# Optimization experiments

Measured on AMD Instinct MI355X. Metric: run time of the kernel, lower is better.

Reference implementation:

```python
import jax, jax.numpy as jnp
import numpy as np

HEADS = 16
DIM = 1024


def setup_inputs() -> dict:
    key = jax.random.key(0)
    ks = jax.random.split(key, 9)
    B, N, D = 2, 2048, DIM
    s = 1.0 / np.sqrt(D)
    x = jax.random.normal(ks[0], (B, N, D), dtype=jnp.float32)
    Wq = jax.random.normal(ks[1], (D, D), dtype=jnp.float32) * s
    Wk = jax.random.normal(ks[2], (D, D), dtype=jnp.float32) * s
    Wv = jax.random.normal(ks[3], (D, D), dtype=jnp.float32) * s
    Wo = jax.random.normal(ks[4], (D, D), dtype=jnp.float32) * s
    bq = jax.random.normal(ks[5], (D,), dtype=jnp.float32) * 0.01
    bk = jax.random.normal(ks[6], (D,), dtype=jnp.float32) * 0.01
    bv = jax.random.normal(ks[7], (D,), dtype=jnp.float32) * 0.01
    bo = jax.random.normal(ks[8], (D,), dtype=jnp.float32) * 0.01
    return {"x": x, "Wq": Wq, "bq": bq, "Wk": Wk, "bk": bk,
            "Wv": Wv, "bv": bv, "Wo": Wo, "bo": bo}


def reference(x, Wq, bq, Wk, bk, Wv, bv, Wo, bo):
    B, N, D = x.shape
    H = HEADS
    hd = D // H
    scale = hd ** (-0.5)
    # projections; split heads -> [B, H, N, hd]
    q = (x @ Wq + bq).reshape(B, N, H, hd).transpose(0, 2, 1, 3)
    k = (x @ Wk + bk).reshape(B, N, H, hd).transpose(0, 2, 1, 3)
    v = (x @ Wv + bv).reshape(B, N, H, hd).transpose(0, 2, 1, 3)
    # full [B, H, N, N] scores (faithful to naive torch implementation)
    attn = jnp.einsum('bhqd,bhkd->bhqk', q, k) * scale
    attn = jax.nn.softmax(attn, axis=-1)
    # dropout is identity in eval mode
    out = jnp.einsum('bhqk,bhkd->bhqd', attn, v)
    out = out.transpose(0, 2, 1, 3).reshape(B, N, D)
    return out @ Wo + bo
```

## Files before the change

kernel.cpp:

```cpp
#include <hip/hip_runtime.h>

#define HEADS 16
#define HD 64
#define SEQ 2048
#define DMODEL 1024
#define BATCH 2
#define MTOT (BATCH*SEQ)
#define KVB 64
#define NKH 16

typedef unsigned short u16;
typedef __bf16 bf16;
typedef bf16 bf16x8 __attribute__((ext_vector_type(8)));
typedef float f32x4 __attribute__((ext_vector_type(4)));
typedef float f32x16 __attribute__((ext_vector_type(16)));
typedef unsigned short u16x8 __attribute__((ext_vector_type(8)));
typedef unsigned short u16x4 __attribute__((ext_vector_type(4)));

static __device__ __forceinline__ u16 f2bf(float f) {
  bf16 b = (bf16)f;
  return __builtin_bit_cast(u16, b);
}

static __device__ __forceinline__ void async16(u16* lds_base, const u16* g) {
  __builtin_amdgcn_global_load_lds(
      (const __attribute__((address_space(1))) unsigned int*)g,
      (__attribute__((address_space(3))) unsigned int*)lds_base,
      16, 0, 0);
}

__global__ __launch_bounds__(256) void k_cvt(const float* __restrict__ in,
                                             u16* __restrict__ out, int n8) {
  int i = blockIdx.x * blockDim.x + threadIdx.x;
  if (i >= n8) return;
  const float4* p = (const float4*)(in + (size_t)i * 8);
  float4 a = p[0], b = p[1];
  u16x8 r;
  r[0] = f2bf(a.x); r[1] = f2bf(a.y); r[2] = f2bf(a.z); r[3] = f2bf(a.w);
  r[4] = f2bf(b.x); r[5] = f2bf(b.y); r[6] = f2bf(b.z); r[7] = f2bf(b.w);
  *(u16x8*)(out + (size_t)i * 8) = r;
}

__global__ __launch_bounds__(256) void k_cvtT(const float* __restrict__ W0, const float* __restrict__ W1,
                                              const float* __restrict__ W2, const float* __restrict__ W3,
                                              u16* __restrict__ T0, u16* __restrict__ T1,
                                              u16* __restrict__ T2, u16* __restrict__ T3) {
  const float* W = blockIdx.z == 0 ? W0 : blockIdx.z == 1 ? W1 : blockIdx.z == 2 ? W2 : W3;
  u16*         T = blockIdx.z == 0 ? T0 : blockIdx.z == 1 ? T1 : blockIdx.z == 2 ? T2 : T3;
  __shared__ u16 tile[64 * 68];
  int t = threadIdx.x;
  int kb = blockIdx.y * 64, nb = blockIdx.x * 64;
#pragma unroll
  for (int i = 0; i < 4; ++i) {
    int c = t * 4 + i;
    int row = c >> 4;
    int c4 = c & 15;
    float4 v = *(const float4*)&W[(size_t)(kb + row) * DMODEL + nb + c4 * 4];
    tile[row * 68 + c4 * 4 + 0] = f2bf(v.x);
    tile[row * 68 + c4 * 4 + 1] = f2bf(v.y);
    tile[row * 68 + c4 * 4 + 2] = f2bf(v.z);
    tile[row * 68 + c4 * 4 + 3] = f2bf(v.w);
  }
  __syncthreads();
#pragma unroll
  for (int i = 0; i < 2; ++i) {
    int c = t * 2 + i;
    int n = c >> 3;
    int k8 = c & 7;
    u16x8 v;
#pragma unroll
    for (int e = 0; e < 8; ++e) v[e] = tile[(k8 * 8 + e) * 68 + n];
    *(u16x8*)&T[(size_t)(nb + n) * DMODEL + kb + k8 * 8] = v;
  }
}

__global__ __launch_bounds__(256) void k_gemm(
    const u16* __restrict__ A,
    const u16* __restrict__ BT0, const u16* __restrict__ BT1, const u16* __restrict__ BT2,
    const float* __restrict__ b0, const float* __restrict__ b1, const float* __restrict__ b2,
    void* __restrict__ O0, void* __restrict__ O1, void* __restrict__ O2,
    int M, int N, int K) {
  const u16* BT = blockIdx.z == 0 ? BT0 : blockIdx.z == 1 ? BT1 : BT2;
  const float* bias = blockIdx.z == 0 ? b0 : blockIdx.z == 1 ? b1 : b2;
  void* Out = blockIdx.z == 0 ? O0 : blockIdx.z == 1 ? O1 : O2;

  __shared__ u16 Ads[2][128 * 32];
  __shared__ u16 Bds[2][128 * 32];
  int tid = threadIdx.x, wid = tid >> 6, lane = tid & 63;
  int r = lane & 15, g = lane >> 4;
  int wm = wid >> 1, wn = wid & 1;
  int m0 = blockIdx.y * 128, n0 = blockIdx.x * 128;

  f32x4 acc[4][4];
  f32x4 zero4 = {0.f, 0.f, 0.f, 0.f};
#pragma unroll
  for (int mt = 0; mt < 4; ++mt)
#pragma unroll
    for (int nt = 0; nt < 4; ++nt) acc[mt][nt] = zero4;

  int srow = lane >> 2;
  int scb = lane & 3;

  auto STAGE = [&](int b, int k0) {
#pragma unroll
    for (int tt = 0; tt < 2; ++tt) {
      int inst = wid * 2 + tt;
      int row = inst * 16 + srow;
      async16(&Ads[b][inst * 512], &A[(size_t)(m0 + row) * K + k0 + scb * 8]);
      async16(&Bds[b][inst * 512], &BT[(size_t)(n0 + row) * K + k0 + scb * 8]);
    }
  };

  auto BODY = [&](int buf, int k0) {
    if (k0 + 32 < K) STAGE(buf ^ 1, k0 + 32);
    bf16x8 af[4], bfv[4];
#pragma unroll
    for (int mt = 0; mt < 4; ++mt)
      af[mt] = *(const bf16x8*)&Ads[buf][(wm * 64 + mt * 16 + r) * 32 + g * 8];
#pragma unroll
    for (int nt = 0; nt < 4; ++nt)
      bfv[nt] = *(const bf16x8*)&Bds[buf][(wn * 64 + nt * 16 + r) * 32 + g * 8];
#pragma unroll
    for (int mt = 0; mt < 4; ++mt)
#pragma unroll
      for (int nt = 0; nt < 4; ++nt)
        acc[mt][nt] = __builtin_amdgcn_mfma_f32_16x16x32_bf16(af[mt], bfv[nt], acc[mt][nt], 0, 0, 0);
    asm volatile("s_waitcnt vmcnt(0)" ::: "memory");
    __builtin_amdgcn_sched_barrier(0);
    __builtin_amdgcn_s_barrier();
    __builtin_amdgcn_sched_barrier(0);
  };

  STAGE(0, 0);
  asm volatile("s_waitcnt vmcnt(0)" ::: "memory");
  __builtin_amdgcn_sched_barrier(0);
  __builtin_amdgcn_s_barrier();
  __builtin_amdgcn_sched_barrier(0);

  for (int k0 = 0; k0 < K; k0 += 64) {
    BODY(0, k0);
    BODY(1, k0 + 32);
  }

  const float qs = 0.18033688011112042f;
#pragma unroll
  for (int nt = 0; nt < 4; ++nt) {
    int col = n0 + wn * 64 + nt * 16 + r;
    float bv = bias[col];
#pragma unroll
    for (int mt = 0; mt < 4; ++mt) {
      int rowb = m0 + wm * 64 + mt * 16 + g * 4;
      int b = rowb >> 11;
      int h = col >> 6, d = col & (HD - 1);
      if (blockIdx.z == 2) {
        int n = rowb & (SEQ - 1);
        int np = (n & ~12) | ((n & 4) << 1) | ((n & 8) >> 1);
        u16x4 pk;
#pragma unroll
        for (int j = 0; j < 4; ++j) pk[j] = f2bf(acc[mt][nt][j] + bv);
        *(u16x4*)&((u16*)Out)[((size_t)((b * HEADS + h) * HD + d)) * SEQ + np] = pk;
      } else {
        float sc = (blockIdx.z == 0) ? qs : 1.0f;
#pragma unroll
        for (int j = 0; j < 4; ++j) {
          int row = rowb + j;
          int n = row & (SEQ - 1);
          ((u16*)Out)[((size_t)(b * HEADS + h) * SEQ + n) * HD + d] = f2bf((acc[mt][nt][j] + bv) * sc);
        }
      }
    }
  }
}

__global__ __launch_bounds__(512, 2) void k_gemm1(
    const u16* __restrict__ A, const u16* __restrict__ BT,
    const float* __restrict__ bias, float* __restrict__ Out,
    int M, int N, int K) {
  __shared__ u16 smem[32768];
  u16* Apart = smem;
  u16* Bpart = smem + 16384;

  int tid = threadIdx.x, wid = tid >> 6, lane = tid & 63;
  int r = lane & 15, g = lane >> 4;
  int h = wid >> 2, w = wid & 3;
  int wm = w >> 1, wn = w & 1;

  int fid = blockIdx.y * gridDim.x + blockIdx.x;
  int nb = (fid & 7) * 32 + (fid >> 3);
  int m0 = (nb >> 3) * 128, n0 = (nb & 7) * 128;

  f32x4 acc[4][4];
  f32x4 zero4 = {0.f, 0.f, 0.f, 0.f};
#pragma unroll
  for (int mt = 0; mt < 4; ++mt)
#pragma unroll
    for (int nt = 0; nt < 4; ++nt) acc[mt][nt] = zero4;

  int srow = lane >> 2;
  int scb = lane & 3;
  const int KH = K >> 1;

  auto STAGE = [&](int b, int k0) {
    int kg = h * KH + k0;
#pragma unroll
    for (int tt = 0; tt < 2; ++tt) {
      int inst = w * 2 + tt;
      int row = inst * 16 + srow;
      async16(&Apart[((b * 2 + h) * 8 + inst) * 512], &A[(size_t)(m0 + row) * K + kg + scb * 8]);
      async16(&Bpart[((b * 2 + h) * 8 + inst) * 512], &BT[(size_t)(n0 + row) * K + kg + scb * 8]);
    }
  };

  auto BODY = [&](int buf, int k0) {
    if (k0 + 32 < KH) STAGE(buf ^ 1, k0 + 32);
    const u16* Ab = &Apart[(buf * 2 + h) * 4096];
    const u16* Bb = &Bpart[(buf * 2 + h) * 4096];
    bf16x8 af[4], bfv[4];
#pragma unroll
    for (int mt = 0; mt < 4; ++mt)
      af[mt] = *(const bf16x8*)&Ab[(wm * 64 + mt * 16 + r) * 32 + g * 8];
#pragma unroll
    for (int nt = 0; nt < 4; ++nt)
      bfv[nt] = *(const bf16x8*)&Bb[(wn * 64 + nt * 16 + r) * 32 + g * 8];
#pragma unroll
    for (int mt = 0; mt < 4; ++mt)
#pragma unroll
      for (int nt = 0; nt < 4; ++nt)
        acc[mt][nt] = __builtin_amdgcn_mfma_f32_16x16x32_bf16(af[mt], bfv[nt], acc[mt][nt], 0, 0, 0);
    asm volatile("s_waitcnt vmcnt(0)" ::: "memory");
    __builtin_amdgcn_sched_barrier(0);
    __builtin_amdgcn_s_barrier();
    __builtin_amdgcn_sched_barrier(0);
  };

  STAGE(0, 0);
  asm volatile("s_waitcnt vmcnt(0)" ::: "memory");
  __builtin_amdgcn_sched_barrier(0);
  __builtin_amdgcn_s_barrier();
  __builtin_amdgcn_sched_barrier(0);

  for (int k0 = 0; k0 < KH; k0 += 64) {
    BODY(0, k0);
    BODY(1, k0 + 32);
  }

  __syncthreads();
  float* cfp = (float*)smem;
  if (h == 1) {
#pragma unroll
    for (int mt = 0; mt < 4; ++mt)
#pragma unroll
      for (int nt = 0; nt < 4; ++nt)
#pragma unroll
        for (int j = 0; j < 4; ++j)
          cfp[(wm * 64 + mt * 16 + g * 4 + j) * 128 + wn * 64 + nt * 16 + r] = acc[mt][nt][j];
  }
  __syncthreads();
  if (h == 0) {
#pragma unroll
    for (int nt = 0; nt < 4; ++nt) {
      int col = n0 + wn * 64 + nt * 16 + r;
      float bv = bias[col];
#pragma unroll
      for (int mt = 0; mt < 4; ++mt) {
        int rowb = m0 + wm * 64 + mt * 16 + g * 4;
#pragma unroll
        for (int j = 0; j < 4; ++j) {
          float v = acc[mt][nt][j] + bv +
                    cfp[(wm * 64 + mt * 16 + g * 4 + j) * 128 + wn * 64 + nt * 16 + r];
          Out[(size_t)(rowb + j) * N + col] = v;
        }
      }
    }
  }
}

__global__ __launch_bounds__(512, 2) void k_attn(const u16* __restrict__ Q,
                                                 const u16* __restrict__ Kg,
                                                 const u16* __restrict__ Vt,
                                                 u16* __restrict__ Oa) {
  __shared__ u16 lds[2][2][2][KVB * 64];

  int tid = threadIdx.x, wid = tid >> 6, lane = tid & 63;
  int l31 = lane & 31, hi = lane >> 5;
  int h = wid >> 2, s = wid & 3;

  int fid = blockIdx.y * gridDim.x + blockIdx.x;
  int swz = (fid & 7) * 32 + (fid >> 3);
  int qt = swz & 7;
  int bh = swz >> 3;

  const size_t kbase = (size_t)bh * SEQ * HD;
  const size_t vbase = (size_t)bh * HD * SEQ;
  int qA = qt * 256 + s * 64;

  bf16x8 qfA[4], qfB[4];
#pragma unroll
  for (int db = 0; db < 4; ++db) {
    qfA[db] = *(const bf16x8*)&Q[kbase + (size_t)(qA + l31) * HD + db * 16 + hi * 8];
    qfB[db] = *(const bf16x8*)&Q[kbase + (size_t)(qA + 32 + l31) * HD + db * 16 + hi * 8];
  }

  int swz7 = l31 & 7;
  int coff[4];
#pragma unroll
  for (int i = 0; i < 4; ++i) coff[i] = ((2 * i + hi) ^ swz7) * 8;

  f32x16 zero16 = {0.f,0.f,0.f,0.f,0.f,0.f,0.f,0.f,0.f,0.f,0.f,0.f,0.f,0.f,0.f,0.f};
  f32x16 oa0A = zero16, oa1A = zero16, lA = zero16;
  f32x16 oa0B = zero16, oa1B = zero16, lB = zero16;

  u16x8 onesb;
#pragma unroll
  for (int e = 0; e < 8; ++e) onesb[e] = 0x3F80;
  bf16x8 ones = __builtin_bit_cast(bf16x8, onesb);

  auto STAGE = [&](int b, int kc) {
    int kof = (h * NKH + kc) * KVB;
#pragma unroll
    for (int i = 0; i < 2; ++i) {
      int inst = s * 2 + i;
      int rr = inst * 8 + (lane >> 3);
      int ch = (lane & 7) ^ (rr & 7);
      async16(&lds[b][h][0][inst * 512], &Kg[kbase + (size_t)(kof + rr) * HD + ch * 8]);
      async16(&lds[b][h][1][inst * 512], &Vt[vbase + (size_t)rr * SEQ + kof + ch * 8]);
    }
  };

  auto BODY = [&](int buf, int kc) {
    if (kc + 1 < NKH) STAGE(buf ^ 1, kc + 1);

    const u16* Kb = &lds[buf][h][0][0];
    const u16* Vb = &lds[buf][h][1][0];

    f32x16 s0A = zero16, s1A = zero16, s0B = zero16, s1B = zero16;
#pragma unroll
    for (int db = 0; db < 4; ++db) {
      bf16x8 kf0 = *(const bf16x8*)&Kb[l31 * 64 + coff[db]];
      bf16x8 kf1 = *(const bf16x8*)&Kb[2048 + l31 * 64 + coff[db]];
      s0A = __builtin_amdgcn_mfma_f32_32x32x16_bf16(kf0, qfA[db], s0A, 0, 0, 0);
      s1A = __builtin_amdgcn_mfma_f32_32x32x16_bf16(kf1, qfA[db], s1A, 0, 0, 0);
      s0B = __builtin_amdgcn_mfma_f32_32x32x16_bf16(kf0, qfB[db], s0B, 0, 0, 0);
      s1B = __builtin_amdgcn_mfma_f32_32x32x16_bf16(kf1, qfB[db], s1B, 0, 0, 0);
    }

#pragma unroll
    for (int t = 0; t < 4; ++t) {
      u16x8 pkA, pkB;
#pragma unroll
      for (int e = 0; e < 8; ++e) {
        float svA = (t & 2) ? ((t & 1) ? s1A[8 + e] : s1A[e])
                            : ((t & 1) ? s0A[8 + e] : s0A[e]);
        float svB = (t & 2) ? ((t & 1) ? s1B[8 + e] : s1B[e])
                            : ((t & 1) ? s0B[8 + e] : s0B[e]);
        pkA[e] = f2bf(__builtin_amdgcn_exp2f(svA));
        pkB[e] = f2bf(__builtin_amdgcn_exp2f(svB));
      }
      bf16x8 paA = __builtin_bit_cast(bf16x8, pkA);
      bf16x8 paB = __builtin_bit_cast(bf16x8, pkB);

      bf16x8 vf0 = *(const bf16x8*)&Vb[l31 * 64 + coff[t]];
      bf16x8 vf1 = *(const bf16x8*)&Vb[2048 + l31 * 64 + coff[t]];
      lA   = __builtin_amdgcn_mfma_f32_32x32x16_bf16(paA, ones, lA, 0, 0, 0);
      oa0A = __builtin_amdgcn_mfma_f32_32x32x16_bf16(paA, vf0, oa0A, 0, 0, 0);
      oa1A = __builtin_amdgcn_mfma_f32_32x32x16_bf16(paA, vf1, oa1A, 0, 0, 0);
      lB   = __builtin_amdgcn_mfma_f32_32x32x16_bf16(paB, ones, lB, 0, 0, 0);
      oa0B = __builtin_amdgcn_mfma_f32_32x32x16_bf16(paB, vf0, oa0B, 0, 0, 0);
      oa1B = __builtin_amdgcn_mfma_f32_32x32x16_bf16(paB, vf1, oa1B, 0, 0, 0);
    }

    asm volatile("s_waitcnt vmcnt(0)" ::: "memory");
    __builtin_amdgcn_sched_barrier(0);
    __builtin_amdgcn_s_barrier();
    __builtin_amdgcn_sched_barrier(0);
  };

  STAGE(0, 0);
  asm volatile("s_waitcnt vmcnt(0)" ::: "memory");
  __builtin_amdgcn_sched_barrier(0);
  __builtin_amdgcn_s_barrier();
  __builtin_amdgcn_sched_barrier(0);

  for (int kc = 0; kc < NKH; kc += 2) {
    BODY(0, kc);
    BODY(1, kc + 1);
  }

  float* cf = (float*)&lds[0][0][0][0];
  int b = bh >> 4, hh = bh & 15;

  if (h == 1) {
#pragma unroll
    for (int r2 = 0; r2 < 16; ++r2) {
      cf[s * 3072 + r2 * 64 + lane]        = oa0A[r2];
      cf[s * 3072 + 1024 + r2 * 64 + lane] = oa1A[r2];
      cf[s * 3072 + 2048 + r2 * 64 + lane] = lA[r2];
    }
  }
  __syncthreads();
  if (h == 0) {
#pragma unroll
    for (int reg = 0; reg < 16; ++reg) {
      float o0 = oa0A[reg] + cf[s * 3072 + reg * 64 + lane];
      float o1 = oa1A[reg] + cf[s * 3072 + 1024 + reg * 64 + lane];
      float lv = lA[reg]   + cf[s * 3072 + 2048 + reg * 64 + lane];
      float inv = 1.0f / lv;
      int q = qA + (reg & 3) + 8 * (reg >> 2) + 4 * hi;
      size_t rowoff = ((size_t)(b * SEQ + q)) * DMODEL + hh * HD;
      Oa[rowoff + l31]      = f2bf(o0 * inv);
      Oa[rowoff + 32 + l31] = f2bf(o1 * inv);
    }
  }
  __syncthreads();
  if (h == 1) {
#pragma unroll
    for (int r2 = 0; r2 < 16; ++r2) {
      cf[s * 3072 + r2 * 64 + lane]        = oa0B[r2];
      cf[s * 3072 + 1024 + r2 * 64 + lane] = oa1B[r2];
      cf[s * 3072 + 2048 + r2 * 64 + lane] = lB[r2];
    }
  }
  __syncthreads();
  if (h == 0) {
#pragma unroll
    for (int reg = 0; reg < 16; ++reg) {
      float o0 = oa0B[reg] + cf[s * 3072 + reg * 64 + lane];
      float o1 = oa1B[reg] + cf[s * 3072 + 1024 + reg * 64 + lane];
      float lv = lB[reg]   + cf[s * 3072 + 2048 + reg * 64 + lane];
      float inv = 1.0f / lv;
      int q = qA + 32 + (reg & 3) + 8 * (reg >> 2) + 4 * hi;
      size_t rowoff = ((size_t)(b * SEQ + q)) * DMODEL + hh * HD;
      Oa[rowoff + l31]      = f2bf(o0 * inv);
      Oa[rowoff + 32 + l31] = f2bf(o1 * inv);
    }
  }
}

extern "C" void kernel_launch(void* const* d_in, const int* in_sizes, int n_in,
                              void* d_out, int out_size, void* d_ws, size_t ws_size,
                              hipStream_t stream) {
  const float* x  = (const float*)d_in[0];
  const float* Wq = (const float*)d_in[1];
  const float* bq = (const float*)d_in[2];
  const float* Wk = (const float*)d_in[3];
  const float* bk = (const float*)d_in[4];
  const float* Wv = (const float*)d_in[5];
  const float* bv = (const float*)d_in[6];
  const float* Wo = (const float*)d_in[7];
  const float* bo = (const float*)d_in[8];

  char* ws = (char*)d_ws;
  const size_t MB = 1024 * 1024;
  u16* xb    = (u16*)(ws);
  u16* wqT   = (u16*)(ws + 8 * MB);
  u16* wkT   = (u16*)(ws + 10 * MB);
  u16* wvT   = (u16*)(ws + 12 * MB);
  u16* woT   = (u16*)(ws + 14 * MB);
  u16* qbuf  = (u16*)(ws + 16 * MB);
  u16* kbuf  = (u16*)(ws + 24 * MB);
  u16* vbufT = (u16*)(ws + 32 * MB);
  u16* abuf  = (u16*)(ws + 40 * MB);

  k_cvt<<<2048, 256, 0, stream>>>(x, xb, (MTOT * DMODEL) / 8);
  k_cvtT<<<dim3(16, 16, 4), 256, 0, stream>>>(Wq, Wk, Wv, Wo, wqT, wkT, wvT, woT);
  k_gemm<<<dim3(DMODEL / 128, MTOT / 128, 3), 256, 0, stream>>>(
      xb, wqT, wkT, wvT, bq, bk, bv, qbuf, kbuf, vbufT, MTOT, DMODEL, DMODEL);
  k_attn<<<dim3(SEQ / 256, BATCH * HEADS), 512, 0, stream>>>(qbuf, kbuf, vbufT, abuf);
  k_gemm1<<<dim3(DMODEL / 128, MTOT / 128), 512, 0, stream>>>(
      abuf, woT, bo, (float*)d_out, MTOT, DMODEL, DMODEL);
}
```

Baseline: 105.9 us.

## Triple-buffer LDS staging in GEMM and attention kernels with prefetch distance two

Both the projection GEMM and the attention kernel move from double to triple LDS buffers, prefetching two tiles ahead and waiting with vmcnt(4) so the most recent prefetch can stay in flight across the barrier. This is meant to hide global-to-LDS load latency that was previously exposed by a full vmcnt(0) drain every iteration. It raises LDS use, which in the attention kernel (launch bounds 512,2) may reduce occupancy, and the loops now index buffers with mod 3 rather than being unrolled in pairs.

```diff
diff --git a/kernel.cpp b/kernel.cpp
--- a/kernel.cpp
+++ b/kernel.cpp
@@ -27,6 +27,14 @@
       (const __attribute__((address_space(1))) unsigned int*)g,
       (__attribute__((address_space(3))) unsigned int*)lds_base,
       16, 0, 0);
+}
+
+static __device__ __forceinline__ void wait_vm(bool deep) {
+  if (deep) asm volatile("s_waitcnt vmcnt(4)" ::: "memory");
+  else      asm volatile("s_waitcnt vmcnt(0)" ::: "memory");
+  __builtin_amdgcn_sched_barrier(0);
+  __builtin_amdgcn_s_barrier();
+  __builtin_amdgcn_sched_barrier(0);
 }
 
 __global__ __launch_bounds__(256) void k_cvt(const float* __restrict__ in,
@@ -84,8 +92,8 @@
   const float* bias = blockIdx.z == 0 ? b0 : blockIdx.z == 1 ? b1 : b2;
   void* Out = blockIdx.z == 0 ? O0 : blockIdx.z == 1 ? O1 : O2;
 
-  __shared__ u16 Ads[2][128 * 32];
-  __shared__ u16 Bds[2][128 * 32];
+  __shared__ u16 Ads[3][128 * 32];
+  __shared__ u16 Bds[3][128 * 32];
   int tid = threadIdx.x, wid = tid >> 6, lane = tid & 63;
   int r = lane & 15, g = lane >> 4;
   int wm = wid >> 1, wn = wid & 1;
@@ -111,8 +119,8 @@
     }
   };
 
-  auto BODY = [&](int buf, int k0) {
-    if (k0 + 32 < K) STAGE(buf ^ 1, k0 + 32);
+  auto BODY = [&](int buf, int k0, bool deep) {
+    if (k0 + 64 < K) STAGE((buf + 2) % 3, k0 + 64);
     bf16x8 af[4], bfv[4];
 #pragma unroll
     for (int mt = 0; mt < 4; ++mt)
@@ -125,22 +133,16 @@
 #pragma unroll
       for (int nt = 0; nt < 4; ++nt)
         acc[mt][nt] = __builtin_amdgcn_mfma_f32_16x16x32_bf16(af[mt], bfv[nt], acc[mt][nt], 0, 0, 0);
-    asm volatile("s_waitcnt vmcnt(0)" ::: "memory");
-    __builtin_amdgcn_sched_barrier(0);
-    __builtin_amdgcn_s_barrier();
-    __builtin_amdgcn_sched_barrier(0);
+    wait_vm(deep);
   };
 
   STAGE(0, 0);
-  asm volatile("s_waitcnt vmcnt(0)" ::: "memory");
-  __builtin_amdgcn_sched_barrier(0);
-  __builtin_amdgcn_s_barrier();
-  __builtin_amdgcn_sched_barrier(0);
-
-  for (int k0 = 0; k0 < K; k0 += 64) {
-    BODY(0, k0);
-    BODY(1, k0 + 32);
-  }
+  STAGE(1, 32);
+  wait_vm(true);
+
+  int kc = 0;
+  for (int k0 = 0; k0 < K; k0 += 32, ++kc)
+    BODY(kc % 3, k0, k0 + 64 < K);
 
   const float qs = 0.18033688011112042f;
 #pragma unroll
@@ -279,7 +281,7 @@
                                                  const u16* __restrict__ Kg,
                                                  const u16* __restrict__ Vt,
                                                  u16* __restrict__ Oa) {
-  __shared__ u16 lds[2][2][2][KVB * 64];
+  __shared__ u16 lds[3][2][2][KVB * 64];
 
   int tid = threadIdx.x, wid = tid >> 6, lane = tid & 63;
   int l31 = lane & 31, hi = lane >> 5;
@@ -327,8 +329,8 @@
     }
   };
 
-  auto BODY = [&](int buf, int kc) {
-    if (kc + 1 < NKH) STAGE(buf ^ 1, kc + 1);
+  auto BODY = [&](int buf, int kc, bool deep) {
+    if (kc + 2 < NKH) STAGE((buf + 2) % 3, kc + 2);
 
     const u16* Kb = &lds[buf][h][0][0];
     const u16* Vb = &lds[buf][h][1][0];
@@ -369,22 +371,15 @@
       oa1B = __builtin_amdgcn_mfma_f32_32x32x16_bf16(paB, vf1, oa1B, 0, 0, 0);
     }
 
-    asm volatile("s_waitcnt vmcnt(0)" ::: "memory");
-    __builtin_amdgcn_sched_barrier(0);
-    __builtin_amdgcn_s_barrier();
-    __builtin_amdgcn_sched_barrier(0);
+    wait_vm(deep);
   };
 
   STAGE(0, 0);
-  asm volatile("s_waitcnt vmcnt(0)" ::: "memory");
-  __builtin_amdgcn_sched_barrier(0);
-  __builtin_amdgcn_s_barrier();
-  __builtin_amdgcn_sched_barrier(0);
-
-  for (int kc = 0; kc < NKH; kc += 2) {
-    BODY(0, kc);
-    BODY(1, kc + 1);
-  }
+  STAGE(1, 1);
+  wait_vm(true);
+
+  for (int kc = 0; kc < NKH; ++kc)
+    BODY(kc % 3, kc, kc + 2 < NKH);
 
   float* cf = (float*)&lds[0][0][0][0];
   int b = bh >> 4, hh = bh & 15;
```

After: 106.6 us. No clear change (+0.6%).
